# Performance work log

Hardware: AMD Instinct MI355X
Metric: run time of the kernel (lower is better)

Reference implementation:

```python
import jax, jax.numpy as jnp
import numpy as np

B, T, C, H = 2, 2048, 1024, 16
D = C // H  # head dim


def setup_inputs() -> dict:
    key = jax.random.key(0)
    k1, k2, k3 = jax.random.split(key, 3)
    x = jax.random.normal(k1, (B, T, C), dtype=jnp.float32)
    w_qkv = jax.random.normal(k2, (3 * C, C), dtype=jnp.float32) * (1.0 / np.sqrt(C))
    b_qkv = jnp.zeros((3 * C,), dtype=jnp.float32)
    w_proj = jax.random.normal(k3, (C, C), dtype=jnp.float32) * (1.0 / np.sqrt(C))
    b_proj = jnp.zeros((C,), dtype=jnp.float32)
    return {"x": x, "w_qkv": w_qkv, "b_qkv": b_qkv, "w_proj": w_proj, "b_proj": b_proj}


def reference(x, w_qkv, b_qkv, w_proj, b_proj):
    # torch Linear: y = x @ W^T + b
    qkv = jnp.einsum('btc,oc->bto', x, w_qkv) + b_qkv  # [B,T,3C]
    q, k, v = jnp.split(qkv, 3, axis=-1)
    # [B,T,C] -> [B,H,T,D]
    reshape = lambda t: t.reshape(B, T, H, D).transpose(0, 2, 1, 3)
    q, k, v = reshape(q), reshape(k), reshape(v)
    scale = 1.0 / jnp.sqrt(jnp.float32(C))  # NOTE: full C, as in source
    att = jnp.einsum('bhtd,bhsd->bhts', q, k) * scale  # [B,H,T,T]
    causal = jnp.tril(jnp.ones((T, T), dtype=bool))
    att = jnp.where(causal, att, -jnp.inf)
    att = jax.nn.softmax(att, axis=-1)
    y = jnp.einsum('bhts,bhsd->bhtd', att, v)  # [B,H,T,D]
    y = y.transpose(0, 2, 1, 3).reshape(B, T, C)
    return jnp.einsum('btc,oc->bto', y, w_proj) + b_proj
```

## Files before the change

### kernel.cpp

```cpp
#include <hip/hip_runtime.h>

#define DEVINL __device__ __forceinline__

typedef __attribute__((ext_vector_type(8))) short short8;
typedef __attribute__((ext_vector_type(4))) float f32x4;

DEVINL unsigned f2bf_u(float x) {
  union { float f; unsigned u; } v; v.f = x;
  unsigned r = v.u + 0x7FFF + ((v.u >> 16) & 1);
  return r >> 16;
}
DEVINL unsigned short f2bf(float x) { return (unsigned short)f2bf_u(x); }

DEVINL unsigned cvt_pk_bf16(float lo, float hi) {
  unsigned r;
  asm("v_cvt_pk_bf16_f32 %0, %1, %2" : "=v"(r) : "v"(lo), "v"(hi));
  return r;
}

#if __has_builtin(__builtin_amdgcn_exp2f)
#define EXP2(x) __builtin_amdgcn_exp2f(x)
#else
#define EXP2(x) exp2f(x)
#endif

DEVINL void gload_lds16(const void* g, void* l) {
  __builtin_amdgcn_global_load_lds(
      (const __attribute__((address_space(1))) unsigned int*)g,
      (__attribute__((address_space(3))) unsigned int*)l, 16, 0, 0);
}

DEVINL short8 as_s8(uint4 v) { union { uint4 u; short8 s; } c; c.u = v; return c.s; }
DEVINL f32x4 fzero() { f32x4 z = {0.f, 0.f, 0.f, 0.f}; return z; }

__global__ __launch_bounds__(256) void cvt3_kernel(
    const float4* __restrict__ x, const float4* __restrict__ wq,
    const float4* __restrict__ wp, ushort4* __restrict__ xo,
    ushort4* __restrict__ wqo, ushort4* __restrict__ wpo) {
  const int N1 = 1048576, N2 = 1835008, NT = 2097152;
  int i = blockIdx.x * blockDim.x + threadIdx.x;
  int stride = gridDim.x * blockDim.x;
  for (; i < NT; i += stride) {
    const float4* s; ushort4* d; int j;
    if (i < N1) { s = x; d = xo; j = i; }
    else if (i < N2) { s = wq; d = wqo; j = i - N1; }
    else { s = wp; d = wpo; j = i - N2; }
    float4 v = s[j];
    ushort4 o;
    o.x = f2bf(v.x); o.y = f2bf(v.y); o.z = f2bf(v.z); o.w = f2bf(v.w);
    d[j] = o;
  }
}

template <int MODE, int RX, int RY>
__global__ __launch_bounds__(256, 2) void gemm_bt(
    const ushort* __restrict__ A, const ushort* __restrict__ Bw,
    const float* __restrict__ bias,
    ushort* __restrict__ Qb, ushort* __restrict__ Kb, ushort* __restrict__ Vt,
    float* __restrict__ Out, int M, int N, int K) {
  __shared__ __align__(16) char smem[32768];
  char* ldsA = smem;
  char* ldsB = smem + 16384;

  int gx = gridDim.x;
  int id = blockIdx.y * gx + blockIdx.x;
  int xcd = id & 7, slot = id >> 3;
  int rw = gx / RX, rh = gridDim.y / RY;
  int bx = (xcd % RX) * rw + slot % rw;
  int by = (xcd / RX) * rh + slot / rw;

  int m0 = by * 128, n0 = bx * 128;
  int t = threadIdx.x;
  int lane = t & 63, w = t >> 6;
  int q = lane & 15, g = lane >> 4;
  int wr = w >> 1, wc = w & 1;

  int Lrow[4], Lcol[4];
#pragma unroll
  for (int i = 0; i < 4; ++i) {
    int L = i * 4096 + t * 16;
    int row = L >> 7, c = L & 127;
    Lrow[i] = row;
    Lcol[i] = c ^ ((row & 7) << 4);
  }
  const char* Abase = (const char*)A + (size_t)m0 * K * 2;
  const char* Bbase = (const char*)Bw + (size_t)n0 * K * 2;

  f32x4 acc[4][4];
#pragma unroll
  for (int i = 0; i < 4; ++i)
#pragma unroll
    for (int j = 0; j < 4; ++j) acc[i][j] = fzero();

  for (int k0 = 0; k0 < K; k0 += 64) {
    __syncthreads();
#pragma unroll
    for (int i = 0; i < 4; ++i) {
      int L = i * 4096 + t * 16;
      gload_lds16(Abase + (size_t)Lrow[i] * (K * 2) + k0 * 2 + Lcol[i], ldsA + L);
    }
#pragma unroll
    for (int i = 0; i < 4; ++i) {
      int L = i * 4096 + t * 16;
      gload_lds16(Bbase + (size_t)Lrow[i] * (K * 2) + k0 * 2 + Lcol[i], ldsB + L);
    }
    __syncthreads();

    uint4 bf[2][4];
#pragma unroll
    for (int s = 0; s < 2; ++s)
#pragma unroll
      for (int nt = 0; nt < 4; ++nt) {
        int row = wc * 64 + nt * 16 + q;
        int addr = row * 128 + ((g * 16 + 64 * s) ^ ((row & 7) << 4));
        bf[s][nt] = *(const uint4*)(ldsB + addr);
      }
#pragma unroll
    for (int mt = 0; mt < 4; ++mt) {
      int row = wr * 64 + mt * 16 + q;
      int a0 = row * 128 + ((g * 16) ^ ((row & 7) << 4));
      int a1 = row * 128 + ((g * 16 + 64) ^ ((row & 7) << 4));
      uint4 af0 = *(const uint4*)(ldsA + a0);
      uint4 af1 = *(const uint4*)(ldsA + a1);
#pragma unroll
      for (int nt = 0; nt < 4; ++nt) {
        acc[mt][nt] = __builtin_amdgcn_mfma_f32_16x16x32_bf16(
            as_s8(af0), as_s8(bf[0][nt]), acc[mt][nt], 0, 0, 0);
        acc[mt][nt] = __builtin_amdgcn_mfma_f32_16x16x32_bf16(
            as_s8(af1), as_s8(bf[1][nt]), acc[mt][nt], 0, 0, 0);
      }
    }
  }

  if (MODE == 0) {
    int mrow0 = m0 + wr * 64;
    int b = mrow0 >> 11, tt0 = mrow0 & 2047;
    if (n0 >= 2048) {
      int hs = (n0 + wc * 64) >> 6;
      int h = hs & 15;
      ushort* vb = Vt + ((size_t)(b * 16 + h) * 64) * 2048;
#pragma unroll
      for (int nt = 0; nt < 4; ++nt) {
        int d = nt * 16 + q;
        float bv = bias[n0 + wc * 64 + nt * 16 + q];
#pragma unroll
        for (int mt = 0; mt < 4; ++mt) {
          uint2 o;
          o.x = cvt_pk_bf16(acc[mt][nt][0] + bv, acc[mt][nt][1] + bv);
          o.y = cvt_pk_bf16(acc[mt][nt][2] + bv, acc[mt][nt][3] + bv);
          *(uint2*)(vb + (size_t)d * 2048 + tt0 + mt * 16 + g * 4) = o;
        }
      }
    } else {
      __syncthreads();
      char* tile = smem + w * 8192;
      float bv[4];
#pragma unroll
      for (int nt = 0; nt < 4; ++nt) bv[nt] = bias[n0 + wc * 64 + nt * 16 + q];
#pragma unroll
      for (int mt = 0; mt < 4; ++mt)
#pragma unroll
        for (int nt = 0; nt < 4; ++nt)
#pragma unroll
          for (int r = 0; r < 4; ++r) {
            int row = mt * 16 + g * 4 + r;
            int bcol = ((nt * 16 + q) * 2) ^ ((row & 7) << 4);
            *(ushort*)(tile + row * 128 + bcol) = f2bf(acc[mt][nt][r] + bv[nt]);
          }
      int hs = (n0 + wc * 64) >> 6;
      int which = hs >> 4, h = hs & 15;
      ushort* dst = which == 0 ? Qb : Kb;
      ushort* dbase = dst + (size_t)(b * 16 + h) * 131072 + (size_t)tt0 * 64;
#pragma unroll
      for (int p = 0; p < 8; ++p) {
        int row = p * 8 + (lane >> 3);
        int bcol = ((lane & 7) * 16) ^ ((row & 7) << 4);
        uint4 v = *(const uint4*)(tile + row * 128 + bcol);
        *(uint4*)(dbase + (size_t)row * 64 + (lane & 7) * 8) = v;
      }
    }
  } else {
#pragma unroll
    for (int nt = 0; nt < 4; ++nt) {
      int ncol = n0 + wc * 64 + nt * 16 + q;
      float bv = bias[ncol];
#pragma unroll
      for (int mt = 0; mt < 4; ++mt)
#pragma unroll
        for (int r = 0; r < 4; ++r) {
          int m = m0 + wr * 64 + mt * 16 + g * 4 + r;
          Out[(size_t)m * N + ncol] = acc[mt][nt][r] + bv;
        }
    }
  }
}

__global__ __launch_bounds__(512, 1) void attn_kernel(
    const ushort* __restrict__ Q, const ushort* __restrict__ K,
    const ushort* __restrict__ Vt, ushort* __restrict__ Y) {
  __shared__ __align__(16) char smem[65536];
  const float C44 = 0.0450842298f;
  const float THR44 = 11.5415603f;
  int id = blockIdx.x;
  int xcd = id & 7, slot = id >> 3;
  int bh = xcd * 4 + (slot >> 4);
  int pidx = slot & 15;
  int t = threadIdx.x;
  int lane = t & 63, w = t >> 6;
  int q = lane & 15, g = lane >> 4;
  int wq = w & 3, half = w >> 2;
  int b = bh >> 4, hh = bh & 15;

  const char* Kc0 = (const char*)(K + (size_t)bh * 2048 * 64);
  const char* Vc0 = (const char*)(Vt + (size_t)bh * 64 * 2048);

  int krow[2], kcol[2], vrow[2], vcol[2];
#pragma unroll
  for (int i = 0; i < 2; ++i) {
    int L = i * 8192 + t * 16;
    krow[i] = L >> 7;
    kcol[i] = (L & 127) ^ ((krow[i] & 7) << 4);
    vrow[i] = L >> 8;
    vcol[i] = (L & 255) ^ ((vrow[i] & 7) << 4);
  }
  int offK[4][2], offV[4][2];
#pragma unroll
  for (int sub = 0; sub < 4; ++sub)
#pragma unroll
    for (int s = 0; s < 2; ++s) {
      offK[sub][s] = (half * 64 + sub * 16 + q) * 128 +
                     ((g * 16 + 64 * s) ^ ((q & 7) << 4));
      offV[sub][s] = 16384 + (sub * 16 + q) * 256 +
                     ((half * 128 + g * 16 + 64 * s) ^ ((q & 7) << 4));
    }

#pragma unroll 1
  for (int pass = 0; pass < 2; ++pass) {
    int qt = pass ? pidx : 31 - pidx;
    int nch = (qt >> 1) + 1;
    int qbase = qt * 64;
    int qrow0 = qbase + wq * 16;
    int qg = qrow0 + q;

    uint4 qf[2];
    {
      const ushort* Qrow = Q + ((size_t)bh * 2048 + qrow0 + q) * 64;
      qf[0] = *(const uint4*)(Qrow + g * 8);
      qf[1] = *(const uint4*)(Qrow + 32 + g * 8);
    }

    f32x4 oacc[4];
#pragma unroll
    for (int i = 0; i < 4; ++i) oacc[i] = fzero();
    float m_run = -1e30f;
    float l_run = 0.f;

#pragma unroll
    for (int i = 0; i < 2; ++i) {
      int L = i * 8192 + t * 16;
      gload_lds16(Kc0 + (size_t)krow[i] * 128 + kcol[i], smem + L);
      gload_lds16(Vc0 + (size_t)vrow[i] * 4096 + vcol[i], smem + 16384 + L);
    }
    __syncthreads();

    int cur = 0;
#pragma unroll 1
    for (int c = 0; c < nch; ++c) {
      int kv0 = c * 128;
      if (c + 1 < nch) {
        int kn = kv0 + 128;
        char* dstb = smem + (cur ^ 1) * 32768;
#pragma unroll
        for (int i = 0; i < 2; ++i) {
          int L = i * 8192 + t * 16;
          gload_lds16(Kc0 + (size_t)(kn + krow[i]) * 128 + kcol[i], dstb + L);
          gload_lds16(Vc0 + (size_t)vrow[i] * 4096 + (size_t)kn * 2 + vcol[i],
                      dstb + 16384 + L);
        }
      }
      const char* base = smem + cur * 32768;
      int kst = kv0 + half * 64;
      if (kst <= qrow0 + 15) {
        f32x4 sacc[4];
        __builtin_amdgcn_s_setprio(1);
#pragma unroll
        for (int sub = 0; sub < 4; ++sub) {
          sacc[sub] = fzero();
#pragma unroll
          for (int s = 0; s < 2; ++s)
            sacc[sub] = __builtin_amdgcn_mfma_f32_16x16x32_bf16(
                as_s8(*(const uint4*)(base + offK[sub][s])), as_s8(qf[s]),
                sacc[sub], 0, 0, 0);
        }
        __builtin_amdgcn_s_setprio(0);

        float sr[4][4];
        if (kst + 63 > qrow0) {
#pragma unroll
          for (int sub = 0; sub < 4; ++sub)
#pragma unroll
            for (int r = 0; r < 4; ++r) {
              int kv = kst + sub * 16 + g * 4 + r;
              sr[sub][r] = (kv > qg) ? -3e38f : sacc[sub][r];
            }
        } else {
#pragma unroll
          for (int sub = 0; sub < 4; ++sub)
#pragma unroll
            for (int r = 0; r < 4; ++r) sr[sub][r] = sacc[sub][r];
        }
        float ms[4];
#pragma unroll
        for (int sub = 0; sub < 4; ++sub)
          ms[sub] = fmaxf(fmaxf(sr[sub][0], sr[sub][1]),
                          fmaxf(sr[sub][2], sr[sub][3]));
        float mx44 = fmaxf(fmaxf(ms[0], ms[1]), fmaxf(ms[2], ms[3])) * C44;

        if (!__all(mx44 <= m_run + THR44)) {
          mx44 = fmaxf(mx44, __shfl_xor(mx44, 16));
          mx44 = fmaxf(mx44, __shfl_xor(mx44, 32));
          float mnew = fmaxf(m_run, mx44);
          float corr = EXP2(m_run - mnew);
          float cr[4];
#pragma unroll
          for (int r = 0; r < 4; ++r) cr[r] = __shfl(corr, g * 4 + r);
#pragma unroll
          for (int ds = 0; ds < 4; ++ds)
#pragma unroll
            for (int r = 0; r < 4; ++r) oacc[ds][r] *= cr[r];
          l_run *= corr;
          m_run = mnew;
        }

        float nm = -m_run;
        unsigned pk[4][2];
        float psum = 0.f;
#pragma unroll
        for (int sub = 0; sub < 4; ++sub) {
          float p0 = EXP2(__builtin_fmaf(sr[sub][0], C44, nm));
          float p1 = EXP2(__builtin_fmaf(sr[sub][1], C44, nm));
          float p2 = EXP2(__builtin_fmaf(sr[sub][2], C44, nm));
          float p3 = EXP2(__builtin_fmaf(sr[sub][3], C44, nm));
          psum += (p0 + p1) + (p2 + p3);
          pk[sub][0] = cvt_pk_bf16(p0, p1);
          pk[sub][1] = cvt_pk_bf16(p2, p3);
        }
        l_run += psum;

        uint4 pa[2];
#pragma unroll
        for (int h = 0; h < 2; ++h) {
          unsigned wrd[4];
#pragma unroll
          for (int j2 = 0; j2 < 4; ++j2) {
            int src = ((2 * (g & 1) + (j2 >> 1)) << 4) | q;
            unsigned lo = __shfl(pk[2 * h][j2 & 1], src);
            unsigned hi = __shfl(pk[2 * h + 1][j2 & 1], src);
            wrd[j2] = (g >> 1) ? hi : lo;
          }
          pa[h].x = wrd[0]; pa[h].y = wrd[1]; pa[h].z = wrd[2]; pa[h].w = wrd[3];
        }

        __builtin_amdgcn_s_setprio(1);
#pragma unroll
        for (int ds = 0; ds < 4; ++ds)
#pragma unroll
          for (int h = 0; h < 2; ++h)
            oacc[ds] = __builtin_amdgcn_mfma_f32_16x16x32_bf16(
                as_s8(pa[h]), as_s8(*(const uint4*)(base + offV[ds][h])),
                oacc[ds], 0, 0, 0);
        __builtin_amdgcn_s_setprio(0);
      }

      __syncthreads();
      cur ^= 1;
    }

    l_run += __shfl_xor(l_run, 16);
    l_run += __shfl_xor(l_run, 32);
    float* ob = (float*)smem + wq * 1024;
    float* mlb = (float*)(smem + 16384);
    if (half) {
#pragma unroll
      for (int ds = 0; ds < 4; ++ds)
#pragma unroll
        for (int r = 0; r < 4; ++r)
          ob[(g * 4 + r) * 64 + ds * 16 + q] = oacc[ds][r];
      if (g == 0) {
        mlb[wq * 32 + q] = m_run;
        mlb[wq * 32 + 16 + q] = l_run;
      }
    }
    __syncthreads();
    if (!half) {
#pragma unroll
      for (int r = 0; r < 4; ++r) {
        int row = g * 4 + r;
        float mA = __shfl(m_run, row);
        float lA = __shfl(l_run, row);
        float mB = mlb[wq * 32 + row];
        float lB = mlb[wq * 32 + 16 + row];
        float mS = fmaxf(mA, mB);
        float sA = EXP2(mA - mS), sB = EXP2(mB - mS);
        float linv = 1.0f / (lA * sA + lB * sB);
        sA *= linv; sB *= linv;
#pragma unroll
        for (int ds = 0; ds < 4; ++ds) {
          float vB = ob[row * 64 + ds * 16 + q];
          float yv = oacc[ds][r] * sA + vB * sB;
          Y[(size_t)(b * 2048 + qrow0 + row) * 1024 + hh * 64 + ds * 16 + q] =
              f2bf(yv);
        }
      }
    }
    __syncthreads();
  }
}

extern "C" void kernel_launch(void* const* d_in, const int* in_sizes, int n_in,
                              void* d_out, int out_size, void* d_ws, size_t ws_size,
                              hipStream_t stream) {
  const float* x = (const float*)d_in[0];
  const float* w_qkv = (const float*)d_in[1];
  const float* b_qkv = (const float*)d_in[2];
  const float* w_proj = (const float*)d_in[3];
  const float* b_proj = (const float*)d_in[4];
  float* out = (float*)d_out;
  char* ws = (char*)d_ws;
  const size_t MB = 1024 * 1024;
  ushort* xb    = (ushort*)(ws + 0 * MB);
  ushort* wqkvb = (ushort*)(ws + 8 * MB);
  ushort* wprojb= (ushort*)(ws + 14 * MB);
  ushort* Qb    = (ushort*)(ws + 16 * MB);
  ushort* Kb    = (ushort*)(ws + 24 * MB);
  ushort* Vt    = (ushort*)(ws + 40 * MB);
  ushort* Yb    = (ushort*)(ws + 48 * MB);

  cvt3_kernel<<<2048, 256, 0, stream>>>((const float4*)x, (const float4*)w_qkv,
                                        (const float4*)w_proj, (ushort4*)xb,
                                        (ushort4*)wqkvb, (ushort4*)wprojb);
  gemm_bt<0, 2, 4><<<dim3(24, 32), 256, 0, stream>>>(xb, wqkvb, b_qkv, Qb, Kb, Vt,
                                                     nullptr, 4096, 3072, 1024);
  attn_kernel<<<dim3(512), 512, 0, stream>>>(Qb, Kb, Vt, Yb);
  gemm_bt<1, 1, 8><<<dim3(8, 32), 256, 0, stream>>>(Yb, wprojb, b_proj, nullptr,
                                                    nullptr, nullptr, out, 4096,
                                                    1024, 1024);
}
```

Measured before the change: 101.2 us.

## Double-buffer GEMM K loop and split attention KV chunks across four wave groups

The GEMM main loop now keeps two LDS tiles, prefetching the next K slice while MFMAs run on the current one, and raises wave priority around the MFMA block. The attention kernel grows to 1024 threads so each 128-key chunk is split four ways (32 keys per wave group) instead of two. Partial outputs and running max/sum are merged through LDS at the end. The larger LDS footprint and the tight launch bound (1024, 8) may cap registers and cause spills, and the four-way merge adds epilogue work.

```diff
diff --git a/kernel.cpp b/kernel.cpp
--- a/kernel.cpp
+++ b/kernel.cpp
@@ -58,9 +58,7 @@
     const float* __restrict__ bias,
     ushort* __restrict__ Qb, ushort* __restrict__ Kb, ushort* __restrict__ Vt,
     float* __restrict__ Out, int M, int N, int K) {
-  __shared__ __align__(16) char smem[32768];
-  char* ldsA = smem;
-  char* ldsB = smem + 16384;
+  __shared__ __align__(16) char smem[65536];
 
   int gx = gridDim.x;
   int id = blockIdx.y * gx + blockIdx.x;
@@ -92,19 +90,31 @@
 #pragma unroll
     for (int j = 0; j < 4; ++j) acc[i][j] = fzero();
 
-  for (int k0 = 0; k0 < K; k0 += 64) {
-    __syncthreads();
-#pragma unroll
-    for (int i = 0; i < 4; ++i) {
-      int L = i * 4096 + t * 16;
-      gload_lds16(Abase + (size_t)Lrow[i] * (K * 2) + k0 * 2 + Lcol[i], ldsA + L);
-    }
-#pragma unroll
-    for (int i = 0; i < 4; ++i) {
-      int L = i * 4096 + t * 16;
-      gload_lds16(Bbase + (size_t)Lrow[i] * (K * 2) + k0 * 2 + Lcol[i], ldsB + L);
-    }
-    __syncthreads();
+#pragma unroll
+  for (int i = 0; i < 4; ++i) {
+    int L = i * 4096 + t * 16;
+    gload_lds16(Abase + (size_t)Lrow[i] * (K * 2) + Lcol[i], smem + L);
+    gload_lds16(Bbase + (size_t)Lrow[i] * (K * 2) + Lcol[i], smem + 16384 + L);
+  }
+  __syncthreads();
+
+  int cur = 0;
+  int nks = K >> 6;
+#pragma unroll 1
+  for (int ks = 0; ks < nks; ++ks) {
+    if (ks + 1 < nks) {
+      int k0 = (ks + 1) * 64;
+      char* dst = smem + (cur ^ 1) * 32768;
+#pragma unroll
+      for (int i = 0; i < 4; ++i) {
+        int L = i * 4096 + t * 16;
+        gload_lds16(Abase + (size_t)Lrow[i] * (K * 2) + k0 * 2 + Lcol[i], dst + L);
+        gload_lds16(Bbase + (size_t)Lrow[i] * (K * 2) + k0 * 2 + Lcol[i],
+                    dst + 16384 + L);
+      }
+    }
+    const char* ldsA = smem + cur * 32768;
+    const char* ldsB = ldsA + 16384;
 
     uint4 bf[2][4];
 #pragma unroll
@@ -115,6 +125,7 @@
         int addr = row * 128 + ((g * 16 + 64 * s) ^ ((row & 7) << 4));
         bf[s][nt] = *(const uint4*)(ldsB + addr);
       }
+    __builtin_amdgcn_s_setprio(1);
 #pragma unroll
     for (int mt = 0; mt < 4; ++mt) {
       int row = wr * 64 + mt * 16 + q;
@@ -130,6 +141,9 @@
             as_s8(af1), as_s8(bf[1][nt]), acc[mt][nt], 0, 0, 0);
       }
     }
+    __builtin_amdgcn_s_setprio(0);
+    __syncthreads();
+    cur ^= 1;
   }
 
   if (MODE == 0) {
@@ -152,7 +166,6 @@
         }
       }
     } else {
-      __syncthreads();
       char* tile = smem + w * 8192;
       float bv[4];
 #pragma unroll
@@ -195,7 +208,7 @@
   }
 }
 
-__global__ __launch_bounds__(512, 1) void attn_kernel(
+__global__ __launch_bounds__(1024, 8) void attn_kernel(
     const ushort* __restrict__ Q, const ushort* __restrict__ K,
     const ushort* __restrict__ Vt, ushort* __restrict__ Y) {
   __shared__ __align__(16) char smem[65536];
@@ -214,32 +227,31 @@
   const char* Kc0 = (const char*)(K + (size_t)bh * 2048 * 64);
   const char* Vc0 = (const char*)(Vt + (size_t)bh * 64 * 2048);
 
-  int krow[2], kcol[2], vrow[2], vcol[2];
-#pragma unroll
-  for (int i = 0; i < 2; ++i) {
-    int L = i * 8192 + t * 16;
-    krow[i] = L >> 7;
-    kcol[i] = (L & 127) ^ ((krow[i] & 7) << 4);
-    vrow[i] = L >> 8;
-    vcol[i] = (L & 255) ^ ((vrow[i] & 7) << 4);
-  }
-  int offK[4][2], offV[4][2];
-#pragma unroll
-  for (int sub = 0; sub < 4; ++sub)
+  int tb = t * 16;
+  int krow = tb >> 7;
+  int kcol = (tb & 127) ^ ((krow & 7) << 4);
+  int vrow = tb >> 8;
+  int vcol = (tb & 255) ^ ((vrow & 7) << 4);
+
+  int offK[2][2], offV[4];
+#pragma unroll
+  for (int sub = 0; sub < 2; ++sub)
 #pragma unroll
     for (int s = 0; s < 2; ++s) {
-      offK[sub][s] = (half * 64 + sub * 16 + q) * 128 +
-                     ((g * 16 + 64 * s) ^ ((q & 7) << 4));
-      offV[sub][s] = 16384 + (sub * 16 + q) * 256 +
-                     ((half * 128 + g * 16 + 64 * s) ^ ((q & 7) << 4));
-    }
+      int row = half * 32 + sub * 16 + q;
+      offK[sub][s] = row * 128 + ((g * 16 + 64 * s) ^ ((row & 7) << 4));
+    }
+#pragma unroll
+  for (int ds = 0; ds < 4; ++ds) {
+    int row = ds * 16 + q;
+    offV[ds] = 16384 + row * 256 + ((half * 64 + g * 16) ^ ((row & 7) << 4));
+  }
 
 #pragma unroll 1
   for (int pass = 0; pass < 2; ++pass) {
     int qt = pass ? pidx : 31 - pidx;
     int nch = (qt >> 1) + 1;
-    int qbase = qt * 64;
-    int qrow0 = qbase + wq * 16;
+    int qrow0 = qt * 64 + wq * 16;
     int qg = qrow0 + q;
 
     uint4 qf[2];
@@ -255,12 +267,8 @@
     float m_run = -1e30f;
     float l_run = 0.f;
 
-#pragma unroll
-    for (int i = 0; i < 2; ++i) {
-      int L = i * 8192 + t * 16;
-      gload_lds16(Kc0 + (size_t)krow[i] * 128 + kcol[i], smem + L);
-      gload_lds16(Vc0 + (size_t)vrow[i] * 4096 + vcol[i], smem + 16384 + L);
-    }
+    gload_lds16(Kc0 + (size_t)krow * 128 + kcol, smem + tb);
+    gload_lds16(Vc0 + (size_t)vrow * 4096 + vcol, smem + 16384 + tb);
     __syncthreads();
 
     int cur = 0;
@@ -270,21 +278,17 @@
       if (c + 1 < nch) {
         int kn = kv0 + 128;
         char* dstb = smem + (cur ^ 1) * 32768;
-#pragma unroll
-        for (int i = 0; i < 2; ++i) {
-          int L = i * 8192 + t * 16;
-          gload_lds16(Kc0 + (size_t)(kn + krow[i]) * 128 + kcol[i], dstb + L);
-          gload_lds16(Vc0 + (size_t)vrow[i] * 4096 + (size_t)kn * 2 + vcol[i],
-                      dstb + 16384 + L);
-        }
+        gload_lds16(Kc0 + (size_t)(kn + krow) * 128 + kcol, dstb + tb);
+        gload_lds16(Vc0 + (size_t)vrow * 4096 + (size_t)kn * 2 + vcol,
+                    dstb + 16384 + tb);
       }
       const char* base = smem + cur * 32768;
-      int kst = kv0 + half * 64;
+      int kst = kv0 + half * 32;
       if (kst <= qrow0 + 15) {
-        f32x4 sacc[4];
+        f32x4 sacc[2];
         __builtin_amdgcn_s_setprio(1);
 #pragma unroll
-        for (int sub = 0; sub < 4; ++sub) {
+        for (int sub = 0; sub < 2; ++sub) {
           sacc[sub] = fzero();
 #pragma unroll
           for (int s = 0; s < 2; ++s)
@@ -294,27 +298,20 @@
         }
         __builtin_amdgcn_s_setprio(0);
 
-        float sr[4][4];
-        if (kst + 63 > qrow0) {
-#pragma unroll
-          for (int sub = 0; sub < 4; ++sub)
+        if (kst + 31 > qrow0) {
+#pragma unroll
+          for (int sub = 0; sub < 2; ++sub)
 #pragma unroll
             for (int r = 0; r < 4; ++r) {
               int kv = kst + sub * 16 + g * 4 + r;
-              sr[sub][r] = (kv > qg) ? -3e38f : sacc[sub][r];
+              if (kv > qg) sacc[sub][r] = -3e38f;
             }
-        } else {
-#pragma unroll
-          for (int sub = 0; sub < 4; ++sub)
-#pragma unroll
-            for (int r = 0; r < 4; ++r) sr[sub][r] = sacc[sub][r];
-        }
-        float ms[4];
-#pragma unroll
-        for (int sub = 0; sub < 4; ++sub)
-          ms[sub] = fmaxf(fmaxf(sr[sub][0], sr[sub][1]),
-                          fmaxf(sr[sub][2], sr[sub][3]));
-        float mx44 = fmaxf(fmaxf(ms[0], ms[1]), fmaxf(ms[2], ms[3])) * C44;
+        }
+        float ms0 = fmaxf(fmaxf(sacc[0][0], sacc[0][1]),
+                          fmaxf(sacc[0][2], sacc[0][3]));
+        float ms1 = fmaxf(fmaxf(sacc[1][0], sacc[1][1]),
+                          fmaxf(sacc[1][2], sacc[1][3]));
+        float mx44 = fmaxf(ms0, ms1) * C44;
 
         if (!__all(mx44 <= m_run + THR44)) {
           mx44 = fmaxf(mx44, __shfl_xor(mx44, 16));
@@ -333,42 +330,39 @@
         }
 
         float nm = -m_run;
-        unsigned pk[4][2];
+        unsigned pk[2][2];
         float psum = 0.f;
 #pragma unroll
-        for (int sub = 0; sub < 4; ++sub) {
-          float p0 = EXP2(__builtin_fmaf(sr[sub][0], C44, nm));
-          float p1 = EXP2(__builtin_fmaf(sr[sub][1], C44, nm));
-          float p2 = EXP2(__builtin_fmaf(sr[sub][2], C44, nm));
-          float p3 = EXP2(__builtin_fmaf(sr[sub][3], C44, nm));
+        for (int sub = 0; sub < 2; ++sub) {
+          float p0 = EXP2(__builtin_fmaf(sacc[sub][0], C44, nm));
+          float p1 = EXP2(__builtin_fmaf(sacc[sub][1], C44, nm));
+          float p2 = EXP2(__builtin_fmaf(sacc[sub][2], C44, nm));
+          float p3 = EXP2(__builtin_fmaf(sacc[sub][3], C44, nm));
           psum += (p0 + p1) + (p2 + p3);
           pk[sub][0] = cvt_pk_bf16(p0, p1);
           pk[sub][1] = cvt_pk_bf16(p2, p3);
         }
         l_run += psum;
 
-        uint4 pa[2];
-#pragma unroll
-        for (int h = 0; h < 2; ++h) {
+        uint4 pa;
+        {
           unsigned wrd[4];
 #pragma unroll
           for (int j2 = 0; j2 < 4; ++j2) {
-            int src = ((2 * (g & 1) + (j2 >> 1)) << 4) | q;
-            unsigned lo = __shfl(pk[2 * h][j2 & 1], src);
-            unsigned hi = __shfl(pk[2 * h + 1][j2 & 1], src);
+            int src = (((g & 1) * 2 + (j2 >> 1)) << 4) | q;
+            unsigned lo = __shfl(pk[0][j2 & 1], src);
+            unsigned hi = __shfl(pk[1][j2 & 1], src);
             wrd[j2] = (g >> 1) ? hi : lo;
           }
-          pa[h].x = wrd[0]; pa[h].y = wrd[1]; pa[h].z = wrd[2]; pa[h].w = wrd[3];
+          pa.x = wrd[0]; pa.y = wrd[1]; pa.z = wrd[2]; pa.w = wrd[3];
         }
 
         __builtin_amdgcn_s_setprio(1);
 #pragma unroll
         for (int ds = 0; ds < 4; ++ds)
-#pragma unroll
-          for (int h = 0; h < 2; ++h)
-            oacc[ds] = __builtin_amdgcn_mfma_f32_16x16x32_bf16(
-                as_s8(pa[h]), as_s8(*(const uint4*)(base + offV[ds][h])),
-                oacc[ds], 0, 0, 0);
+          oacc[ds] = __builtin_amdgcn_mfma_f32_16x16x32_bf16(
+              as_s8(pa), as_s8(*(const uint4*)(base + offV[ds])),
+              oacc[ds], 0, 0, 0);
         __builtin_amdgcn_s_setprio(0);
       }
 
@@ -378,38 +372,47 @@
 
     l_run += __shfl_xor(l_run, 16);
     l_run += __shfl_xor(l_run, 32);
-    float* ob = (float*)smem + wq * 1024;
-    float* mlb = (float*)(smem + 16384);
+    float* obase = (float*)smem;
+    float* mlb = (float*)(smem + 49152);
     if (half) {
+      float* ob = obase + (wq * 3 + half - 1) * 1024;
 #pragma unroll
       for (int ds = 0; ds < 4; ++ds)
 #pragma unroll
         for (int r = 0; r < 4; ++r)
           ob[(g * 4 + r) * 64 + ds * 16 + q] = oacc[ds][r];
       if (g == 0) {
-        mlb[wq * 32 + q] = m_run;
-        mlb[wq * 32 + 16 + q] = l_run;
+        mlb[(wq * 4 + half) * 32 + q] = m_run;
+        mlb[(wq * 4 + half) * 32 + 16 + q] = l_run;
       }
     }
     __syncthreads();
     if (!half) {
+      const float* ob1 = obase + (wq * 3 + 0) * 1024;
+      const float* ob2 = obase + (wq * 3 + 1) * 1024;
+      const float* ob3 = obase + (wq * 3 + 2) * 1024;
 #pragma unroll
       for (int r = 0; r < 4; ++r) {
         int row = g * 4 + r;
-        float mA = __shfl(m_run, row);
-        float lA = __shfl(l_run, row);
-        float mB = mlb[wq * 32 + row];
-        float lB = mlb[wq * 32 + 16 + row];
-        float mS = fmaxf(mA, mB);
-        float sA = EXP2(mA - mS), sB = EXP2(mB - mS);
-        float linv = 1.0f / (lA * sA + lB * sB);
-        sA *= linv; sB *= linv;
+        float m0v = __shfl(m_run, row);
+        float l0v = __shfl(l_run, row);
+        float m1 = mlb[(wq * 4 + 1) * 32 + row];
+        float l1 = mlb[(wq * 4 + 1) * 32 + 16 + row];
+        float m2 = mlb[(wq * 4 + 2) * 32 + row];
+        float l2 = mlb[(wq * 4 + 2) * 32 + 16 + row];
+        float m3 = mlb[(wq * 4 + 3) * 32 + row];
+        float l3 = mlb[(wq * 4 + 3) * 32 + 16 + row];
+        float mS = fmaxf(fmaxf(m0v, m1), fmaxf(m2, m3));
+        float s0 = EXP2(m0v - mS), s1 = EXP2(m1 - mS);
+        float s2 = EXP2(m2 - mS), s3 = EXP2(m3 - mS);
+        float linv = 1.0f / (l0v * s0 + l1 * s1 + l2 * s2 + l3 * s3);
+        s0 *= linv; s1 *= linv; s2 *= linv; s3 *= linv;
 #pragma unroll
         for (int ds = 0; ds < 4; ++ds) {
-          float vB = ob[row * 64 + ds * 16 + q];
-          float yv = oacc[ds][r] * sA + vB * sB;
-          Y[(size_t)(b * 2048 + qrow0 + row) * 1024 + hh * 64 + ds * 16 + q] =
-              f2bf(yv);
+          int cc = ds * 16 + q;
+          float yv = oacc[ds][r] * s0 + ob1[row * 64 + cc] * s1 +
+                     ob2[row * 64 + cc] * s2 + ob3[row * 64 + cc] * s3;
+          Y[(size_t)(b * 2048 + qrow0 + row) * 1024 + hh * 64 + cc] = f2bf(yv);
         }
       }
     }
@@ -441,7 +444,7 @@
                                         (ushort4*)wqkvb, (ushort4*)wprojb);
   gemm_bt<0, 2, 4><<<dim3(24, 32), 256, 0, stream>>>(xb, wqkvb, b_qkv, Qb, Kb, Vt,
                                                      nullptr, 4096, 3072, 1024);
-  attn_kernel<<<dim3(512), 512, 0, stream>>>(Qb, Kb, Vt, Yb);
+  attn_kernel<<<dim3(512), 1024, 0, stream>>>(Qb, Kb, Vt, Yb);
   gemm_bt<1, 1, 8><<<dim3(8, 32), 256, 0, stream>>>(Yb, wprojb, b_proj, nullptr,
                                                     nullptr, nullptr, out, 4096,
                                                     1024, 1024);
```

Result: slower. 127.4 us (+25.9%).
